# Optimization experiments

Hardware: AMD Instinct MI355X
Metric: run time of the kernel (lower is better)

Reference implementation:

```python
import jax, jax.numpy as jnp
import numpy as np
import math

EMBED_DIM = 128
NUM_HEADS = 8
HEAD_DIM = EMBED_DIM // NUM_HEADS
# Faithful to the source's concat bug: heads [0,1,1,2,3,4,5,6] (head 7 dropped, head 1 duplicated)
HEAD_ORDER = [0, 1, 1, 2, 3, 4, 5, 6]


def setup_inputs() -> dict:
    key = jax.random.key(0)
    ks = jax.random.split(key, 7)
    B, S = 4, 2048
    input_embeddings = jax.random.normal(ks[0], (B, S, EMBED_DIM), dtype=jnp.float32)
    token_attention_masks = jax.random.randint(ks[1], (B, S), 0, 2, dtype=jnp.int64)
    # torch.rand -> uniform [0,1)
    w_query = jax.random.uniform(ks[2], (EMBED_DIM, EMBED_DIM), dtype=jnp.float32)
    w_key = jax.random.uniform(ks[3], (EMBED_DIM, EMBED_DIM), dtype=jnp.float32)
    w_value = jax.random.uniform(ks[4], (EMBED_DIM, EMBED_DIM), dtype=jnp.float32)
    # nn.Linear params
    lim = 1.0 / math.sqrt(EMBED_DIM)
    lin_w = jax.random.uniform(ks[5], (EMBED_DIM, EMBED_DIM), dtype=jnp.float32, minval=-lim, maxval=lim)
    lin_b = jax.random.uniform(ks[6], (EMBED_DIM,), dtype=jnp.float32, minval=-lim, maxval=lim)
    return {"input_embeddings": input_embeddings, "token_attention_masks": token_attention_masks,
            "w_query": w_query, "w_key": w_key, "w_value": w_value, "lin_w": lin_w, "lin_b": lin_b}


def reference(input_embeddings, token_attention_masks, w_query, w_key, w_value, lin_w, lin_b):
    B, S, _ = input_embeddings.shape
    q = input_embeddings @ w_query  # [B,S,D]
    k = input_embeddings @ w_key
    v = input_embeddings @ w_value
    # split heads: [B,S,H,hd] -> [B,H,S,hd]
    qh = q.reshape(B, S, NUM_HEADS, HEAD_DIM).transpose(0, 2, 1, 3)
    kh = k.reshape(B, S, NUM_HEADS, HEAD_DIM).transpose(0, 2, 1, 3)
    vh = v.reshape(B, S, NUM_HEADS, HEAD_DIM).transpose(0, 2, 1, 3)
    # NOTE: source scales by sqrt(full embedding dim), not sqrt(head_dim)
    scale = 1.0 / math.sqrt(EMBED_DIM)
    scores = jnp.einsum('bhsd,bhtd->bhst', qh, kh) * scale  # [B,H,S,S]
    # mask: 0 -> -1000, 1 -> 0; broadcast over query positions
    mask = jnp.where(token_attention_masks == 0, -1000.0, 0.0).astype(scores.dtype)  # [B,S]
    scores = scores + mask[:, None, None, :]
    probs = jax.nn.softmax(scores, axis=-1)
    out_h = jnp.einsum('bhst,bhtd->bhsd', probs, vh)  # [B,H,S,hd]
    # buggy concat order kept faithful
    attn_out = jnp.concatenate([out_h[:, i] for i in HEAD_ORDER], axis=-1)  # [B,S,D]
    return attn_out @ lin_w.T + lin_b
```

## Files before the change

kernel.cpp:

```cpp
#include <hip/hip_runtime.h>
#include <stdint.h>

typedef unsigned short u16;
typedef unsigned int   u32;
typedef int     i32x4  __attribute__((ext_vector_type(4)));
typedef float   f32x4  __attribute__((ext_vector_type(4)));
typedef float   f32x16 __attribute__((ext_vector_type(16)));
typedef __bf16  bf16x8 __attribute__((ext_vector_type(8)));
typedef u32     u32x4  __attribute__((ext_vector_type(4)));
typedef u32     u32x2  __attribute__((ext_vector_type(2)));

union BF8 { bf16x8 v; u16 s[8]; u32x4 q; };

__device__ __forceinline__ u16 f2b_rne(float f) {
    u32 u = __builtin_bit_cast(u32, f);
    u32 r = u + 0x7FFFu + ((u >> 16) & 1u);
    return (u16)(r >> 16);
}
__device__ __forceinline__ u16 f2b_trunc(float f) {
    return (u16)(__builtin_bit_cast(u32, f) >> 16);
}
__device__ __forceinline__ float b2f(u16 h) {
    u32 u = ((u32)h) << 16;
    return __builtin_bit_cast(float, u);
}
__device__ __forceinline__ bf16x8 ld_bf8(const u16* p) {
    BF8 t; t.q = *(const u32x4*)p; return t.v;
}
__device__ __forceinline__ f32x16 zero16() {
    f32x16 z;
#pragma unroll
    for (int i = 0; i < 16; i++) z[i] = 0.f;
    return z;
}
__device__ __forceinline__ f32x4 zero4() {
    f32x4 z;
#pragma unroll
    for (int i = 0; i < 4; i++) z[i] = 0.f;
    return z;
}

#define SCALE2 0.1275312959479341f

__global__ __launch_bounds__(256) void proj_kernel(
    const float* __restrict__ x, const float* __restrict__ wq,
    const float* __restrict__ wk, const float* __restrict__ wv,
    const int* __restrict__ mask, int* __restrict__ Larr,
    u16* Qph, u16* Qpl, u16* Kph, u16* Kpl, u16* VT)
{
    int typ  = blockIdx.y;
    int ct   = threadIdx.x >> 6;
    int lane = threadIdx.x & 63;
    int m = lane & 31, kg = lane >> 5;
    int r0 = blockIdx.x * 32;
    int c = ct * 32 + m;
    int b = r0 >> 11, sl = r0 & 2047;

    __shared__ int pos_sh[32];
    __shared__ int Lsh;

    if (typ != 0) {
        if (threadIdx.x < 64) {
            int tl = threadIdx.x;
            const int* mp = mask + b * 2048 + tl * 32;
            int mv[32]; int cnt = 0;
#pragma unroll
            for (int j4 = 0; j4 < 8; j4++) {
                i32x4 t = *(const i32x4*)(mp + j4 * 4);
#pragma unroll
                for (int q = 0; q < 4; q++) {
                    mv[j4 * 4 + q] = t[q];
                    cnt += (t[q] != 0);
                }
            }
            int off = cnt;
#pragma unroll
            for (int d = 1; d < 64; d <<= 1) {
                int o = __shfl_up(off, d, 64);
                if (tl >= d) off += o;
            }
            if (tl == 63) Lsh = off;
            if (tl == (sl >> 5)) {
                int p = off - cnt;
#pragma unroll
                for (int j = 0; j < 32; j++) {
                    pos_sh[j] = mv[j] ? p : -1;
                    p += (mv[j] != 0);
                }
            }
        }
        __syncthreads();
    }

    const float* wp = (typ == 0) ? wq : (typ == 1) ? wk : wv;

    f32x16 acc = zero16();
#pragma unroll 4
    for (int kk = 0; kk < 128; kk += 16) {
        const float* xp = x + (size_t)(r0 + m) * 128 + kk + kg * 8;
        f32x4 x0 = *(const f32x4*)xp;
        f32x4 x1 = *(const f32x4*)(xp + 4);
        BF8 ah, al;
#pragma unroll
        for (int j = 0; j < 4; j++) {
            u16 hb = f2b_trunc(x0[j]);
            ah.s[j] = hb; al.s[j] = f2b_trunc(x0[j] - b2f(hb));
            u16 hb2 = f2b_trunc(x1[j]);
            ah.s[4 + j] = hb2; al.s[4 + j] = f2b_trunc(x1[j] - b2f(hb2));
        }
        const float* wcol = wp + (size_t)(kk + kg * 8) * 128 + c;
        if (typ < 2) {
            BF8 bh, bl_;
#pragma unroll
            for (int j = 0; j < 8; j++) {
                float w = wcol[(size_t)j * 128];
                u16 hb = f2b_trunc(w);
                bh.s[j] = hb; bl_.s[j] = f2b_trunc(w - b2f(hb));
            }
            acc = __builtin_amdgcn_mfma_f32_32x32x16_bf16(ah.v, bh.v, acc, 0, 0, 0);
            acc = __builtin_amdgcn_mfma_f32_32x32x16_bf16(ah.v, bl_.v, acc, 0, 0, 0);
            acc = __builtin_amdgcn_mfma_f32_32x32x16_bf16(al.v, bh.v, acc, 0, 0, 0);
        } else {
            BF8 bh;
#pragma unroll
            for (int j = 0; j < 8; j++) bh.s[j] = f2b_rne(wcol[(size_t)j * 128]);
            acc = __builtin_amdgcn_mfma_f32_32x32x16_bf16(ah.v, bh.v, acc, 0, 0, 0);
        }
    }

    int hh = c >> 4, d = c & 15;
    if (typ == 0) {
        if (hh == 7) return;
        size_t hb_off = (size_t)(b * 8 + hh) * 2048 * 16 + d;
#pragma unroll
        for (int r = 0; r < 16; r++) {
            int row = (r & 3) + 8 * (r >> 2) + 4 * kg;
            float v = acc[r] * SCALE2;
            u16 hi = f2b_trunc(v);
            size_t idx = hb_off + (size_t)(sl + row) * 16;
            Qph[idx] = hi;
            Qpl[idx] = f2b_trunc(v - b2f(hi));
        }
    } else if (typ == 1) {
        if (hh == 7) return;
        size_t hb_off = (size_t)(b * 8 + hh) * 2048 * 16 + d;
#pragma unroll
        for (int r = 0; r < 16; r++) {
            int row = (r & 3) + 8 * (r >> 2) + 4 * kg;
            int p = pos_sh[row];
            if (p < 0) continue;
            float v = acc[r];
            u16 hi = f2b_trunc(v);
            size_t idx = hb_off + (size_t)p * 16;
            Kph[idx] = hi;
            Kpl[idx] = f2b_trunc(v - b2f(hi));
        }
    } else {
        if (hh != 7) {
#pragma unroll
            for (int rg = 0; rg < 4; rg++) {
#pragma unroll
                for (int q = 0; q < 4; q++) {
                    int row = rg * 8 + 4 * kg + q;
                    int p = pos_sh[row];
                    if (p >= 0)
                        VT[(size_t)(b * 128 + c) * 2048 + p] = f2b_rne(acc[rg * 4 + q]);
                }
            }
        }
        int L = Lsh;
        int npad = (L + 127) & ~127; if (npad < 128) npad = 128;
        int padn = npad - L;
        int slice = blockIdx.x & 63;
        if (padn > 0) {
            int e = slice * 256 + threadIdx.x;
            int k = e & 127, cc = e >> 7;
            if (k < padn) VT[(size_t)(b * 128 + cc) * 2048 + (L + k)] = 0;
        }
        if (slice == 0 && threadIdx.x == 0) Larr[b] = L;
    }
}

__global__ __launch_bounds__(256, 7) void attn_kernel(
    const u16* __restrict__ Qph, const u16* __restrict__ Qpl,
    const u16* __restrict__ Kph, const u16* __restrict__ Kpl,
    const u16* __restrict__ VT, const int* __restrict__ Larr, u16* AO)
{
    __shared__ char smem[9216];
    u16*   pbuf  = (u16*)smem;
    float* obuf  = (float*)smem;
    float* lbuf  = (float*)(smem + 8192);
    float* lsmax = (float*)(smem + 8704);

    int bid = blockIdx.x;
    int bh = bid % 28;
    int qt = bid / 28;
    int b = bh / 7, h = bh % 7;
    int wave = threadIdx.x >> 6, lane = threadIdx.x & 63;
    int m = lane & 31, kg = lane >> 5;
    int qs = qt * 32;

    int L = Larr[b];
    int npad = (L + 127) & ~127; if (npad < 128) npad = 128;
    int kpw = npad >> 2;
    int t0 = wave * kpw, tend = t0 + kpw;

    size_t headoff = (size_t)(b * 8 + h) * 2048 * 16;
    bf16x8 qfh = ld_bf8(Qph + headoff + (size_t)(qs + m) * 16 + kg * 8);
    bf16x8 qfl = ld_bf8(Qpl + headoff + (size_t)(qs + m) * 16 + kg * 8);
    const u16* kbh = Kph + headoff;
    const u16* kbl = Kpl + headoff;

    float mloc = -3.0e38f;
    {
        bf16x8 khc = ld_bf8(kbh + (size_t)(t0 + m) * 16 + kg * 8);
        for (int t = t0; t < tend; t += 32) {
            int tn = (t + 32 < tend) ? (t + 32) : t0;
            bf16x8 khn = ld_bf8(kbh + (size_t)(tn + m) * 16 + kg * 8);
            f32x16 sc = __builtin_amdgcn_mfma_f32_32x32x16_bf16(khc, qfh, zero16(), 0, 0, 0);
            if (t + 32 <= L) {
#pragma unroll
                for (int r = 0; r < 16; r++) mloc = fmaxf(mloc, sc[r]);
            } else {
#pragma unroll
                for (int r = 0; r < 16; r++) {
                    int key = t + (r & 3) + 8 * (r >> 2) + 4 * kg;
                    if (key < L) mloc = fmaxf(mloc, sc[r]);
                }
            }
            khc = khn;
        }
    }
    mloc = fmaxf(mloc, __shfl_xor(mloc, 32, 64));
    if (kg == 0) lsmax[m * 4 + wave] = mloc;
    __syncthreads();
    f32x4 mv = *(const f32x4*)(lsmax + m * 4);
    float mrow = fmaxf(fmaxf(mv[0], mv[1]), fmaxf(mv[2], mv[3]));

    f32x4 o0 = zero4(), o1 = zero4(), l0 = zero4(), l1 = zero4();
    BF8 onesu;
#pragma unroll
    for (int j = 0; j < 8; j++) onesu.s[j] = 0x3F80;
    bf16x8 ones = onesu.v;

    int q16 = lane & 15, krow = lane >> 4;
    const u16* vtb = VT + (size_t)(b * 128 + h * 16 + q16) * 2048;
    int msw = (m >> 1) & 3;
    int qsw = (q16 >> 1) & 3;
    u16* pwb = pbuf + wave * 1024 + m * 32 + kg * 4;
    const u16* pr0 = pbuf + wave * 1024 + q16 * 32 + ((krow ^ qsw) * 8);
    const u16* pr1 = pr0 + 16 * 32;

    bf16x8 khc = ld_bf8(kbh + (size_t)(t0 + m) * 16 + kg * 8);
    bf16x8 klc = ld_bf8(kbl + (size_t)(t0 + m) * 16 + kg * 8);

    for (int t = t0; t < tend; t += 32) {
        int tn = (t + 32 < tend) ? (t + 32) : t0;
        bf16x8 khn = ld_bf8(kbh + (size_t)(tn + m) * 16 + kg * 8);
        bf16x8 kln = ld_bf8(kbl + (size_t)(tn + m) * 16 + kg * 8);
        bf16x8 vf  = ld_bf8(vtb + t + krow * 8);

        f32x16 sc = zero16();
        sc = __builtin_amdgcn_mfma_f32_32x32x16_bf16(khc, qfl, sc, 0, 0, 0);
        sc = __builtin_amdgcn_mfma_f32_32x32x16_bf16(klc, qfh, sc, 0, 0, 0);
        sc = __builtin_amdgcn_mfma_f32_32x32x16_bf16(khc, qfh, sc, 0, 0, 0);
        bool tail = (t + 32 > L);
#pragma unroll
        for (int rg = 0; rg < 4; rg++) {
            float e0 = __builtin_amdgcn_exp2f(sc[rg * 4 + 0] - mrow);
            float e1 = __builtin_amdgcn_exp2f(sc[rg * 4 + 1] - mrow);
            float e2 = __builtin_amdgcn_exp2f(sc[rg * 4 + 2] - mrow);
            float e3 = __builtin_amdgcn_exp2f(sc[rg * 4 + 3] - mrow);
            if (tail) {
                int kb = t + rg * 8 + kg * 4;
                e0 = (kb + 0 < L) ? e0 : 0.f;
                e1 = (kb + 1 < L) ? e1 : 0.f;
                e2 = (kb + 2 < L) ? e2 : 0.f;
                e3 = (kb + 3 < L) ? e3 : 0.f;
            }
            u32x2 pk;
            pk[0] = __builtin_amdgcn_perm(__builtin_bit_cast(u32, e1),
                                          __builtin_bit_cast(u32, e0), 0x07060302u);
            pk[1] = __builtin_amdgcn_perm(__builtin_bit_cast(u32, e3),
                                          __builtin_bit_cast(u32, e2), 0x07060302u);
            *(u32x2*)(pwb + ((rg ^ msw) * 8)) = pk;
        }
        bf16x8 p0 = *(const bf16x8*)pr0;
        bf16x8 p1 = *(const bf16x8*)pr1;
        o0 = __builtin_amdgcn_mfma_f32_16x16x32_bf16(p0, vf, o0, 0, 0, 0);
        o1 = __builtin_amdgcn_mfma_f32_16x16x32_bf16(p1, vf, o1, 0, 0, 0);
        l0 = __builtin_amdgcn_mfma_f32_16x16x32_bf16(p0, ones, l0, 0, 0, 0);
        l1 = __builtin_amdgcn_mfma_f32_16x16x32_bf16(p1, ones, l1, 0, 0, 0);
        khc = khn; klc = kln;
    }

    __syncthreads();

    *(f32x4*)(obuf + wave * 512 + q16 * 32 + krow * 4)      = o0;
    *(f32x4*)(obuf + wave * 512 + q16 * 32 + krow * 4 + 16) = o1;
    if (q16 == 0) {
        *(f32x4*)(lbuf + wave * 32 + krow * 4)      = l0;
        *(f32x4*)(lbuf + wave * 32 + krow * 4 + 16) = l1;
    }
    __syncthreads();

    int dd = threadIdx.x & 15, q = threadIdx.x >> 4;
    int slot0 = (h == 0) ? 0 : h + 1;
#pragma unroll
    for (int hf = 0; hf < 2; hf++) {
        int qq = q + hf * 16;
        float os = obuf[0 * 512 + dd * 32 + qq] + obuf[1 * 512 + dd * 32 + qq]
                 + obuf[2 * 512 + dd * 32 + qq] + obuf[3 * 512 + dd * 32 + qq];
        float ls = lbuf[0 * 32 + qq] + lbuf[1 * 32 + qq]
                 + lbuf[2 * 32 + qq] + lbuf[3 * 32 + qq];
        u16 vb = f2b_rne(os * __builtin_amdgcn_rcpf(ls));
        int orow = b * 2048 + qs + qq;
        AO[orow * 128 + slot0 * 16 + dd] = vb;
        if (h == 1) AO[orow * 128 + 16 + dd] = vb;
    }
}

__global__ __launch_bounds__(256) void fin_kernel(
    const u16* __restrict__ AO, const float* __restrict__ lw,
    const float* __restrict__ lb, float* out)
{
    int ct   = threadIdx.x >> 6;
    int lane = threadIdx.x & 63;
    int m = lane & 31, kg = lane >> 5;
    int r0 = blockIdx.x * 32;
    int c = ct * 32 + m;

    f32x16 acc = zero16();
#pragma unroll 4
    for (int kk = 0; kk < 128; kk += 16) {
        bf16x8 af = ld_bf8(AO + (size_t)(r0 + m) * 128 + kk + kg * 8);
        const float* wp = lw + (size_t)c * 128 + kk + kg * 8;
        f32x4 w0 = *(const f32x4*)wp;
        f32x4 w1 = *(const f32x4*)(wp + 4);
        BF8 bfr;
#pragma unroll
        for (int j = 0; j < 4; j++) {
            bfr.s[j]     = f2b_rne(w0[j]);
            bfr.s[4 + j] = f2b_rne(w1[j]);
        }
        acc = __builtin_amdgcn_mfma_f32_32x32x16_bf16(af, bfr.v, acc, 0, 0, 0);
    }
    float bias = lb[c];
#pragma unroll
    for (int r = 0; r < 16; r++) {
        int row = (r & 3) + 8 * (r >> 2) + 4 * kg;
        out[(size_t)(r0 + row) * 128 + c] = acc[r] + bias;
    }
}

extern "C" void kernel_launch(void* const* d_in, const int* in_sizes, int n_in,
                              void* d_out, int out_size, void* d_ws, size_t ws_size,
                              hipStream_t stream)
{
    const float* x    = (const float*)d_in[0];
    const int*   mask = (const int*)d_in[1];
    const float* wq   = (const float*)d_in[2];
    const float* wk   = (const float*)d_in[3];
    const float* wv   = (const float*)d_in[4];
    const float* lw   = (const float*)d_in[5];
    const float* lb   = (const float*)d_in[6];
    float* out = (float*)d_out;

    char* ws = (char*)d_ws;
    u16* Qph = (u16*)(ws + 0 * 2097152);
    u16* Qpl = (u16*)(ws + 1 * 2097152);
    u16* Kph = (u16*)(ws + 2 * 2097152);
    u16* Kpl = (u16*)(ws + 3 * 2097152);
    u16* VT  = (u16*)(ws + 4 * 2097152);
    u16* AO  = (u16*)(ws + 5 * 2097152);
    int* Larr = (int*)(ws + 6 * 2097152);

    proj_kernel<<<dim3(256, 3), 256, 0, stream>>>(x, wq, wk, wv, mask, Larr,
                                                  Qph, Qpl, Kph, Kpl, VT);
    attn_kernel<<<1792, 256, 0, stream>>>(Qph, Qpl, Kph, Kpl, VT, Larr, AO);
    fin_kernel<<<256, 256, 0, stream>>>(AO, lw, lb, out);
}
```

Measured before the change: 117.3 us.

## Fuse output projection into attention kernel via last-block ticket counter

Removes the separate final linear-projection kernel. Each attention block bumps an atomic counter for its (batch, query-tile) row group, and the last of the 7 head blocks to finish computes the output projection plus bias for those 32 rows. The counters are reset inside the projection kernel. This saves one kernel launch and the gap between kernels, at the cost of thread fences, an atomic per block, and a serialized tail of work on the last-arriving blocks.

```diff
diff --git a/kernel.cpp b/kernel.cpp
--- a/kernel.cpp
+++ b/kernel.cpp
@@ -45,7 +45,7 @@
 __global__ __launch_bounds__(256) void proj_kernel(
     const float* __restrict__ x, const float* __restrict__ wq,
     const float* __restrict__ wk, const float* __restrict__ wv,
-    const int* __restrict__ mask, int* __restrict__ Larr,
+    const int* __restrict__ mask, int* __restrict__ Larr, int* __restrict__ cnt,
     u16* Qph, u16* Qpl, u16* Kph, u16* Kpl, u16* VT)
 {
     int typ  = blockIdx.y;
@@ -56,6 +56,8 @@
     int c = ct * 32 + m;
     int b = r0 >> 11, sl = r0 & 2047;
 
+    if (typ == 0 && threadIdx.x == 0) cnt[blockIdx.x] = 0;
+
     __shared__ int pos_sh[32];
     __shared__ int Lsh;
 
@@ -63,17 +65,17 @@
         if (threadIdx.x < 64) {
             int tl = threadIdx.x;
             const int* mp = mask + b * 2048 + tl * 32;
-            int mv[32]; int cnt = 0;
+            int mv[32]; int cntv = 0;
 #pragma unroll
             for (int j4 = 0; j4 < 8; j4++) {
                 i32x4 t = *(const i32x4*)(mp + j4 * 4);
 #pragma unroll
                 for (int q = 0; q < 4; q++) {
                     mv[j4 * 4 + q] = t[q];
-                    cnt += (t[q] != 0);
+                    cntv += (t[q] != 0);
                 }
             }
-            int off = cnt;
+            int off = cntv;
 #pragma unroll
             for (int d = 1; d < 64; d <<= 1) {
                 int o = __shfl_up(off, d, 64);
@@ -81,7 +83,7 @@
             }
             if (tl == 63) Lsh = off;
             if (tl == (sl >> 5)) {
-                int p = off - cnt;
+                int p = off - cntv;
 #pragma unroll
                 for (int j = 0; j < 32; j++) {
                     pos_sh[j] = mv[j] ? p : -1;
@@ -184,9 +186,12 @@
 __global__ __launch_bounds__(256, 7) void attn_kernel(
     const u16* __restrict__ Qph, const u16* __restrict__ Qpl,
     const u16* __restrict__ Kph, const u16* __restrict__ Kpl,
-    const u16* __restrict__ VT, const int* __restrict__ Larr, u16* AO)
+    const u16* __restrict__ VT, const int* __restrict__ Larr,
+    const float* __restrict__ lw, const float* __restrict__ lb,
+    int* __restrict__ cnt, u16* AO, float* out)
 {
     __shared__ char smem[9216];
+    __shared__ int ticket;
     u16*   pbuf  = (u16*)smem;
     float* obuf  = (float*)smem;
     float* lbuf  = (float*)(smem + 8192);
@@ -318,25 +323,24 @@
         AO[orow * 128 + slot0 * 16 + dd] = vb;
         if (h == 1) AO[orow * 128 + 16 + dd] = vb;
     }
-}
-
-__global__ __launch_bounds__(256) void fin_kernel(
-    const u16* __restrict__ AO, const float* __restrict__ lw,
-    const float* __restrict__ lb, float* out)
-{
-    int ct   = threadIdx.x >> 6;
-    int lane = threadIdx.x & 63;
-    int m = lane & 31, kg = lane >> 5;
-    int r0 = blockIdx.x * 32;
-    int c = ct * 32 + m;
-
+
+    __threadfence();
+    __syncthreads();
+    if (threadIdx.x == 0) ticket = atomicAdd(&cnt[b * 64 + qt], 1);
+    __syncthreads();
+    if (ticket != 6) return;
+    __threadfence();
+
+    int ct2 = threadIdx.x >> 6;
+    int c = ct2 * 32 + m;
+    int r0 = b * 2048 + qs;
     f32x16 acc = zero16();
 #pragma unroll 4
     for (int kk = 0; kk < 128; kk += 16) {
         bf16x8 af = ld_bf8(AO + (size_t)(r0 + m) * 128 + kk + kg * 8);
-        const float* wp = lw + (size_t)c * 128 + kk + kg * 8;
-        f32x4 w0 = *(const f32x4*)wp;
-        f32x4 w1 = *(const f32x4*)(wp + 4);
+        const float* wp2 = lw + (size_t)c * 128 + kk + kg * 8;
+        f32x4 w0 = *(const f32x4*)wp2;
+        f32x4 w1 = *(const f32x4*)(wp2 + 4);
         BF8 bfr;
 #pragma unroll
         for (int j = 0; j < 4; j++) {
@@ -374,9 +378,10 @@
     u16* VT  = (u16*)(ws + 4 * 2097152);
     u16* AO  = (u16*)(ws + 5 * 2097152);
     int* Larr = (int*)(ws + 6 * 2097152);
-
-    proj_kernel<<<dim3(256, 3), 256, 0, stream>>>(x, wq, wk, wv, mask, Larr,
+    int* cnt  = (int*)(ws + 6 * 2097152 + 1024);
+
+    proj_kernel<<<dim3(256, 3), 256, 0, stream>>>(x, wq, wk, wv, mask, Larr, cnt,
                                                   Qph, Qpl, Kph, Kpl, VT);
-    attn_kernel<<<1792, 256, 0, stream>>>(Qph, Qpl, Kph, Kpl, VT, Larr, AO);
-    fin_kernel<<<256, 256, 0, stream>>>(AO, lw, lb, out);
-}
+    attn_kernel<<<1792, 256, 0, stream>>>(Qph, Qpl, Kph, Kpl, VT, Larr,
+                                          lw, lb, cnt, AO, out);
+}
```

After: 335.6 us. 186% more time.
